# Kernel tuning notes

Measured on AMD Instinct MI355X. Metric: run time of the kernel, lower is better.

Reference implementation:

```python
import jax, jax.numpy as jnp
import numpy as np

GAMMA_EPS = 0.05
ALPHA_POS = 4.0
ALPHA_NEG = 1.0

N, D, K_CLUSTERS = 262144, 128, 256


def setup_inputs() -> dict:
    key = jax.random.key(0)
    k1, k2, k3 = jax.random.split(key, 3)
    Xemb = jax.random.normal(k1, (N, D), dtype=jnp.float32)
    scores = jax.random.normal(k2, (N, K_CLUSTERS), dtype=jnp.float32)
    labels = jax.random.randint(k3, (N,), 0, K_CLUSTERS, dtype=jnp.int64)
    h_bias = jnp.asarray(0.1, dtype=jnp.float32)  # nn.Parameter(init_bias)
    return {"Xemb": Xemb, "scores": scores, "labels": labels,
            "h_bias": h_bias, "K": K_CLUSTERS}


def _bcl_forward(Xemb, scores, h_bias, labels, K):
    # labels are uniform in [0, K), so sorted unique labels == arange(K)
    # and the loop's k-index equals the label itself (pos_idx = labels).
    bias = jax.nn.softplus(h_bias)
    pos_bias = bias
    neg_bias = 9.0 * bias + GAMMA_EPS

    # scatter-mean centroids per cluster, then L2-normalize each centroid
    sums = jax.ops.segment_sum(Xemb, labels, num_segments=K)          # [K, D]
    counts = jax.ops.segment_sum(jnp.ones((Xemb.shape[0],), Xemb.dtype),
                                 labels, num_segments=K)              # [K]
    centroids = sums / counts[:, None]
    centroids = centroids / jnp.linalg.norm(centroids, axis=1, keepdims=True)

    x2 = jnp.sum(Xemb * Xemb, axis=1, keepdims=True)                  # [N, 1]
    c2 = jnp.sum(centroids * centroids, axis=1)                       # [K]
    XC_dist = x2 + c2[None, :] - 2.0 * (Xemb @ centroids.T)           # [N, K]

    # positive distance: gather own-cluster column
    pos_distances = jnp.take_along_axis(XC_dist, labels[:, None], axis=1)[:, 0]
    pos_sample_loss = jax.nn.relu(pos_distances - pos_bias)

    # min over negative clusters (exclude own column)
    own = jax.nn.one_hot(labels, K, dtype=jnp.bool_)
    min_neg = jnp.min(jnp.where(own, jnp.inf, XC_dist), axis=1)
    neg_sample_loss = jax.nn.relu(neg_bias - min_neg)

    pos_loss = jnp.mean(pos_sample_loss) * ALPHA_POS
    neg_loss = jnp.mean(neg_sample_loss) * ALPHA_NEG
    return jnp.stack([pos_loss, neg_loss])  # [ctrd_pos, ctrd_neg]


def reference(Xemb, scores, labels, h_bias, K):
    return _bcl_forward(Xemb, scores, h_bias, labels, K)
```

## Files before the change

kernel.cpp:

```cpp
#include <hip/hip_runtime.h>
#include <hip/hip_bf16.h>

#define DD 128
#define KK 256
#define TS 256
#define ROWB 136
#define SPB1 1024

typedef __attribute__((ext_vector_type(8))) short short8;
typedef __attribute__((ext_vector_type(4))) float f32x4;

static __device__ __forceinline__ unsigned short f2bf(float f) {
    unsigned int u = __float_as_uint(f);
    return (unsigned short)((u + 0x7fffu + ((u >> 16) & 1u)) >> 16);
}
static __device__ __forceinline__ float bf2f(unsigned short h) {
    return __uint_as_float(((unsigned int)h) << 16);
}

template<int MODE>
__global__ __launch_bounds__(1024) void k_stage1_gather(
    const float* __restrict__ X, const int* __restrict__ labels,
    float* __restrict__ partial)
{
    __shared__ int lab[SPB1];
    __shared__ int idx[SPB1];
    __shared__ int hist[KK];
    __shared__ int start[KK + 1];
    __shared__ int cursor[KK];

    const int tid  = threadIdx.x;
    const int lane = tid & 63;
    const int wave = tid >> 6;
    const int base = blockIdx.x * SPB1;

    if (tid < KK) hist[tid] = 0;
    __syncthreads();
    {
        const int l = labels[base + tid];
        lab[tid] = l;
        atomicAdd(&hist[l], 1);
    }
    __syncthreads();
    if (wave == 0) {
        const int h0 = hist[4*lane], h1 = hist[4*lane+1];
        const int h2 = hist[4*lane+2], h3 = hist[4*lane+3];
        const int s = h0 + h1 + h2 + h3;
        int t = s;
#pragma unroll
        for (int d = 1; d < 64; d <<= 1) { const int u = __shfl_up(t, d); if (lane >= d) t += u; }
        const int e = t - s;
        start[4*lane]   = e;
        start[4*lane+1] = e + h0;
        start[4*lane+2] = e + h0 + h1;
        start[4*lane+3] = e + h0 + h1 + h2;
        if (lane == 63) start[KK] = t;
    }
    __syncthreads();
    if (tid < KK) cursor[tid] = start[tid];
    __syncthreads();
    {
        const int pos = atomicAdd(&cursor[lab[tid]], 1);
        idx[pos] = tid;
    }
    __syncthreads();

    const int c1 = (wave << 4) + 16;
    int c = wave << 4;
    const int s0 = start[c], s1 = start[c1];
    const int cnt = s1 - s0;

    float2 pf[8];
#pragma unroll
    for (int j = 0; j < 8; ++j)
        if (j < cnt)
            pf[j] = *(const float2*)(X + (size_t)(base + idx[s0 + j]) * DD + 2 * lane);

    float2 acc = make_float2(0.f, 0.f);
    int i = 0;
    for (; i + 8 <= cnt; i += 8) {
#pragma unroll
        for (int j = 0; j < 8; ++j) {
            const float2 v = pf[j];
            if (i + j + 8 < cnt)
                pf[j] = *(const float2*)(X + (size_t)(base + idx[s0 + i + j + 8]) * DD + 2 * lane);
            while (s0 + i + j >= start[c + 1]) {
                if (MODE == 2) {
                    atomicAdd(&partial[(size_t)c * DD + 2*lane],     acc.x);
                    atomicAdd(&partial[(size_t)c * DD + 2*lane + 1], acc.y);
                } else {
                    *(float2*)(partial + ((size_t)blockIdx.x * KK + c) * DD + 2*lane) = acc;
                }
                acc = make_float2(0.f, 0.f); ++c;
            }
            acc.x += v.x; acc.y += v.y;
        }
    }
#pragma unroll
    for (int j = 0; j < 8; ++j) {
        if (i + j < cnt) {
            const float2 v = pf[j];
            while (s0 + i + j >= start[c + 1]) {
                if (MODE == 2) {
                    atomicAdd(&partial[(size_t)c * DD + 2*lane],     acc.x);
                    atomicAdd(&partial[(size_t)c * DD + 2*lane + 1], acc.y);
                } else {
                    *(float2*)(partial + ((size_t)blockIdx.x * KK + c) * DD + 2*lane) = acc;
                }
                acc = make_float2(0.f, 0.f); ++c;
            }
            acc.x += v.x; acc.y += v.y;
        }
    }
    while (c < c1) {
        if (MODE == 2) {
            atomicAdd(&partial[(size_t)c * DD + 2*lane],     acc.x);
            atomicAdd(&partial[(size_t)c * DD + 2*lane + 1], acc.y);
        } else {
            *(float2*)(partial + ((size_t)blockIdx.x * KK + c) * DD + 2*lane) = acc;
        }
        acc = make_float2(0.f, 0.f); ++c;
    }
}

__global__ void k_stage2(const float* __restrict__ partial, int nparts,
                         unsigned short* __restrict__ centb)
{
    const int k = blockIdx.x;
    const int t = threadIdx.x;
    const int d = t & (DD - 1);
    const int slice = t >> 7;
    float s = 0.f;
    for (int b = slice; b < nparts; b += 4)
        s += partial[((size_t)b * KK + k) * DD + d];
    __shared__ float red[4][DD];
    red[slice][d] = s;
    __syncthreads();
    float v = 0.f;
    if (t < DD) v = red[0][d] + red[1][d] + red[2][d] + red[3][d];
    float sq = v * v;
#pragma unroll
    for (int m = 32; m > 0; m >>= 1) sq += __shfl_xor(sq, m);
    __shared__ float wsum[8];
    if ((t & 63) == 0) wsum[t >> 6] = sq;
    __syncthreads();
    if (t < DD) centb[k * DD + d] = f2bf(v * rsqrtf(wsum[0] + wsum[1]));
}

__global__ __launch_bounds__(1024, 4) void k_stage3(
    const float* __restrict__ Xf, const int* __restrict__ labels,
    const unsigned short* __restrict__ centb,
    const float* __restrict__ hbias, float* __restrict__ loss, int spb)
{
    __shared__ unsigned short Cl[KK * ROWB];
    __shared__ unsigned short Xl[TS * ROWB];
    __shared__ int   labs[TS];
    __shared__ float lred[32];

    const int tid = threadIdx.x;
    const float hb = *hbias;
    const float bias = (hb > 20.f) ? hb : log1pf(__expf(hb));
    const float pos_bias = bias;
    const float neg_bias = 9.f * bias + 0.05f;

    const uint4* csrc = (const uint4*)centb;
    for (int c = tid; c < KK * DD / 8; c += 1024) {
        const int row = c >> 4;
        const int col = (c & 15) << 3;
        *(uint4*)(&Cl[row * ROWB + col]) = csrc[c];
    }

    const int lane = tid & 63;
    const int wave = tid >> 6;
    const int m15  = lane & 15;
    const int q    = lane >> 4;
    const int kq   = q << 3;
    const int base = blockIdx.x * spb;
    float pos_acc = 0.f, neg_acc = 0.f;

    for (int t0 = 0; t0 < spb; t0 += TS) {
        __syncthreads();
        const float4* xsrc = (const float4*)(Xf + (size_t)(base + t0) * DD);
        for (int c = tid; c < TS * DD / 4; c += 1024) {
            const int row = c >> 5;
            const int col = (c & 31) << 2;
            const float4 v = xsrc[c];
            ushort4 pk = make_ushort4(f2bf(v.x), f2bf(v.y), f2bf(v.z), f2bf(v.w));
            *(ushort4*)(&Xl[row * ROWB + col]) = pk;
        }
        if (tid < TS) labs[tid] = labels[base + t0 + tid];
        __syncthreads();

        short8 afrag[4];
        const int arow = (wave << 4) + m15;
#pragma unroll
        for (int s = 0; s < 4; ++s)
            afrag[s] = *(const short8*)(&Xl[arow * ROWB + (s << 5) + kq]);

        float x2p = 0.f;
#pragma unroll
        for (int s = 0; s < 4; ++s)
#pragma unroll
            for (int j = 0; j < 8; ++j) {
                const float e = bf2f((unsigned short)afrag[s][j]);
                x2p = fmaf(e, e, x2p);
            }
        x2p += __shfl_xor(x2p, 16);
        x2p += __shfl_xor(x2p, 32);

        f32x4 acc[16];
#pragma unroll
        for (int t = 0; t < 16; ++t) acc[t] = (f32x4){0.f, 0.f, 0.f, 0.f};
#pragma unroll
        for (int t = 0; t < 16; ++t) {
            const int brow = (t << 4) + m15;
#pragma unroll
            for (int s = 0; s < 4; ++s) {
                const short8 bfrag = *(const short8*)(&Cl[brow * ROWB + (s << 5) + kq]);
                acc[t] = __builtin_amdgcn_mfma_f32_16x16x32_bf16(afrag[s], bfrag, acc[t], 0, 0, 0);
            }
        }

#pragma unroll
        for (int r = 0; r < 4; ++r) {
            const int ml = (wave << 4) + (q << 2) + r;
            const int l  = labs[ml];
            const float x2 = __shfl(x2p, (q << 2) + r, 16);
            float posd = -1e30f, negd = -1e30f;
#pragma unroll
            for (int t = 0; t < 16; ++t) {
                const int cl = (t << 4) + m15;
                const float v = acc[t][r];
                const bool isp = (cl == l);
                posd = isp ? v : posd;
                negd = isp ? negd : fmaxf(negd, v);
            }
#pragma unroll
            for (int m = 1; m < 16; m <<= 1) {
                posd = fmaxf(posd, __shfl_xor(posd, m));
                negd = fmaxf(negd, __shfl_xor(negd, m));
            }
            if (m15 == 0) {
                const float pd = x2 + 1.0f - 2.f * posd;
                const float nd = x2 + 1.0f - 2.f * negd;
                pos_acc += fmaxf(pd - pos_bias, 0.f);
                neg_acc += fmaxf(neg_bias - nd, 0.f);
            }
        }
    }

#pragma unroll
    for (int m = 32; m > 0; m >>= 1) {
        pos_acc += __shfl_xor(pos_acc, m);
        neg_acc += __shfl_xor(neg_acc, m);
    }
    if (lane == 0) { lred[wave] = pos_acc; lred[16 + wave] = neg_acc; }
    __syncthreads();
    if (tid == 0) {
        float p = 0.f, n = 0.f;
#pragma unroll
        for (int w = 0; w < 16; ++w) { p += lred[w]; n += lred[16 + w]; }
        atomicAdd(&loss[0], p);
        atomicAdd(&loss[1], n);
    }
}

__global__ void k_final(const float* __restrict__ loss, float* __restrict__ out, float invN)
{
    if (threadIdx.x == 0) {
        out[0] = 4.0f * loss[0] * invN;
        out[1] = loss[1] * invN;
    }
}

extern "C" void kernel_launch(void* const* d_in, const int* in_sizes, int n_in,
                              void* d_out, int out_size, void* d_ws, size_t ws_size,
                              hipStream_t stream)
{
    const float* X      = (const float*)d_in[0];
    const int*   labels = (const int*)d_in[2];
    const float* hbias  = (const float*)d_in[3];
    float* out = (float*)d_out;
    const int N = in_sizes[0] / DD;
    const int G = N / SPB1;

    char* ws = (char*)d_ws;
    const size_t offC    = 256;
    const size_t offPart = offC + (size_t)KK * DD * 2;
    const size_t szPart  = (size_t)G * KK * DD * 4;

    float*          loss    = (float*)ws;
    unsigned short* centb   = (unsigned short*)(ws + offC);
    float*          partial = (float*)(ws + offPart);

    const int mode   = (ws_size >= offPart + szPart) ? 0 : 2;
    const int nparts = (mode == 2) ? 1 : G;

    hipMemsetAsync(loss, 0, 2 * sizeof(float), stream);
    if (mode == 2) hipMemsetAsync(partial, 0, (size_t)KK * DD * 4, stream);

    if (mode == 0) k_stage1_gather<0><<<G, 1024, 0, stream>>>(X, labels, partial);
    else           k_stage1_gather<2><<<G, 1024, 0, stream>>>(X, labels, partial);

    k_stage2<<<KK, 512, 0, stream>>>(partial, nparts, centb);

    k_stage3<<<G, 1024, 0, stream>>>(X, labels, centb, hbias, loss, N / G);

    k_final<<<1, 64, 0, stream>>>(loss, out, 1.0f / (float)N);
}
```

Before: 466.0 us.

## Load X fragments directly from global with register prefetch, dropping LDS staging

```diff
diff --git a/kernel.cpp b/kernel.cpp
--- a/kernel.cpp
+++ b/kernel.cpp
@@ -69,6 +69,7 @@
     int c = wave << 4;
     const int s0 = start[c], s1 = start[c1];
     const int cnt = s1 - s0;
+    int nx = start[c + 1];
 
     float2 pf[8];
 #pragma unroll
@@ -84,14 +85,14 @@
             const float2 v = pf[j];
             if (i + j + 8 < cnt)
                 pf[j] = *(const float2*)(X + (size_t)(base + idx[s0 + i + j + 8]) * DD + 2 * lane);
-            while (s0 + i + j >= start[c + 1]) {
+            while (s0 + i + j >= nx) {
                 if (MODE == 2) {
                     atomicAdd(&partial[(size_t)c * DD + 2*lane],     acc.x);
                     atomicAdd(&partial[(size_t)c * DD + 2*lane + 1], acc.y);
                 } else {
                     *(float2*)(partial + ((size_t)blockIdx.x * KK + c) * DD + 2*lane) = acc;
                 }
-                acc = make_float2(0.f, 0.f); ++c;
+                acc = make_float2(0.f, 0.f); ++c; nx = start[c + 1];
             }
             acc.x += v.x; acc.y += v.y;
         }
@@ -100,14 +101,14 @@
     for (int j = 0; j < 8; ++j) {
         if (i + j < cnt) {
             const float2 v = pf[j];
-            while (s0 + i + j >= start[c + 1]) {
+            while (s0 + i + j >= nx) {
                 if (MODE == 2) {
                     atomicAdd(&partial[(size_t)c * DD + 2*lane],     acc.x);
                     atomicAdd(&partial[(size_t)c * DD + 2*lane + 1], acc.y);
                 } else {
                     *(float2*)(partial + ((size_t)blockIdx.x * KK + c) * DD + 2*lane) = acc;
                 }
-                acc = make_float2(0.f, 0.f); ++c;
+                acc = make_float2(0.f, 0.f); ++c; nx = start[c + 1];
             }
             acc.x += v.x; acc.y += v.y;
         }
@@ -147,14 +148,43 @@
     if (t < DD) centb[k * DD + d] = f2bf(v * rsqrtf(wsum[0] + wsum[1]));
 }
 
+
+static __device__ __forceinline__ short8 cvt_pair(const f32x4 lo, const f32x4 hi, float& x2p) {
+    short8 r;
+#pragma unroll
+    for (int j = 0; j < 4; ++j) {
+        const unsigned short u = f2bf(lo[j]);
+        r[j] = (short)u;
+        const float e = bf2f(u);
+        x2p = fmaf(e, e, x2p);
+    }
+#pragma unroll
+    for (int j = 0; j < 4; ++j) {
+        const unsigned short u = f2bf(hi[j]);
+        r[4 + j] = (short)u;
+        const float e = bf2f(u);
+        x2p = fmaf(e, e, x2p);
+    }
+    return r;
+}
+
+static __device__ __forceinline__ void mfma_step(
+    f32x4* acc, const short8 afrag, const unsigned short* Cl,
+    const int m15, const int kq, const int s)
+{
+#pragma unroll
+    for (int t = 0; t < 16; ++t) {
+        const short8 bfrag = *(const short8*)(&Cl[((t << 4) + m15) * ROWB + (s << 5) + kq]);
+        acc[t] = __builtin_amdgcn_mfma_f32_16x16x32_bf16(afrag, bfrag, acc[t], 0, 0, 0);
+    }
+}
+
 __global__ __launch_bounds__(1024, 4) void k_stage3(
     const float* __restrict__ Xf, const int* __restrict__ labels,
     const unsigned short* __restrict__ centb,
     const float* __restrict__ hbias, float* __restrict__ loss, int spb)
 {
     __shared__ unsigned short Cl[KK * ROWB];
-    __shared__ unsigned short Xl[TS * ROWB];
-    __shared__ int   labs[TS];
     __shared__ float lred[32];
 
     const int tid = threadIdx.x;
@@ -169,6 +199,7 @@
         const int col = (c & 15) << 3;
         *(uint4*)(&Cl[row * ROWB + col]) = csrc[c];
     }
+    __syncthreads();
 
     const int lane = tid & 63;
     const int wave = tid >> 6;
@@ -178,53 +209,47 @@
     const int base = blockIdx.x * spb;
     float pos_acc = 0.f, neg_acc = 0.f;
 
+    const float* xp = Xf + (size_t)(base + (wave << 4) + m15) * DD + kq;
+
+    f32x4 pa0 = *(const f32x4*)(xp);
+    f32x4 pa1 = *(const f32x4*)(xp + 4);
+    f32x4 pb0, pb1;
+
     for (int t0 = 0; t0 < spb; t0 += TS) {
-        __syncthreads();
-        const float4* xsrc = (const float4*)(Xf + (size_t)(base + t0) * DD);
-        for (int c = tid; c < TS * DD / 4; c += 1024) {
-            const int row = c >> 5;
-            const int col = (c & 31) << 2;
-            const float4 v = xsrc[c];
-            ushort4 pk = make_ushort4(f2bf(v.x), f2bf(v.y), f2bf(v.z), f2bf(v.w));
-            *(ushort4*)(&Xl[row * ROWB + col]) = pk;
-        }
-        if (tid < TS) labs[tid] = labels[base + t0 + tid];
-        __syncthreads();
-
-        short8 afrag[4];
-        const int arow = (wave << 4) + m15;
-#pragma unroll
-        for (int s = 0; s < 4; ++s)
-            afrag[s] = *(const short8*)(&Xl[arow * ROWB + (s << 5) + kq]);
-
+        const float* xt = xp + (size_t)t0 * DD;
+        f32x4 acc[16];
+#pragma unroll
+        for (int t = 0; t < 16; ++t) acc[t] = (f32x4){0.f, 0.f, 0.f, 0.f};
         float x2p = 0.f;
-#pragma unroll
-        for (int s = 0; s < 4; ++s)
-#pragma unroll
-            for (int j = 0; j < 8; ++j) {
-                const float e = bf2f((unsigned short)afrag[s][j]);
-                x2p = fmaf(e, e, x2p);
-            }
+        short8 afrag;
+
+        afrag = cvt_pair(pa0, pa1, x2p);
+        pb0 = *(const f32x4*)(xt + 32);
+        pb1 = *(const f32x4*)(xt + 36);
+        mfma_step(acc, afrag, Cl, m15, kq, 0);
+        afrag = cvt_pair(pb0, pb1, x2p);
+        pa0 = *(const f32x4*)(xt + 64);
+        pa1 = *(const f32x4*)(xt + 68);
+        mfma_step(acc, afrag, Cl, m15, kq, 1);
+        afrag = cvt_pair(pa0, pa1, x2p);
+        pb0 = *(const f32x4*)(xt + 96);
+        pb1 = *(const f32x4*)(xt + 100);
+        mfma_step(acc, afrag, Cl, m15, kq, 2);
+        afrag = cvt_pair(pb0, pb1, x2p);
+        if (t0 + TS < spb) {
+            const float* xn = xt + (size_t)TS * DD;
+            pa0 = *(const f32x4*)(xn);
+            pa1 = *(const f32x4*)(xn + 4);
+        }
+        mfma_step(acc, afrag, Cl, m15, kq, 3);
+
         x2p += __shfl_xor(x2p, 16);
         x2p += __shfl_xor(x2p, 32);
 
-        f32x4 acc[16];
-#pragma unroll
-        for (int t = 0; t < 16; ++t) acc[t] = (f32x4){0.f, 0.f, 0.f, 0.f};
-#pragma unroll
-        for (int t = 0; t < 16; ++t) {
-            const int brow = (t << 4) + m15;
-#pragma unroll
-            for (int s = 0; s < 4; ++s) {
-                const short8 bfrag = *(const short8*)(&Cl[brow * ROWB + (s << 5) + kq]);
-                acc[t] = __builtin_amdgcn_mfma_f32_16x16x32_bf16(afrag[s], bfrag, acc[t], 0, 0, 0);
-            }
-        }
-
 #pragma unroll
         for (int r = 0; r < 4; ++r) {
             const int ml = (wave << 4) + (q << 2) + r;
-            const int l  = labs[ml];
+            const int l  = labels[base + t0 + ml];
             const float x2 = __shfl(x2p, (q << 2) + r, 16);
             float posd = -1e30f, negd = -1e30f;
 #pragma unroll
```

Result: slower. 705.4 us (+51.4%).

## Register-prefetch next X tile, reorder MFMA loop, and read labels directly

Applied to the files above, without the earlier changes.

```diff
diff --git a/kernel.cpp b/kernel.cpp
--- a/kernel.cpp
+++ b/kernel.cpp
@@ -69,6 +69,7 @@
     int c = wave << 4;
     const int s0 = start[c], s1 = start[c1];
     const int cnt = s1 - s0;
+    int nx = start[c + 1];
 
     float2 pf[8];
 #pragma unroll
@@ -84,14 +85,14 @@
             const float2 v = pf[j];
             if (i + j + 8 < cnt)
                 pf[j] = *(const float2*)(X + (size_t)(base + idx[s0 + i + j + 8]) * DD + 2 * lane);
-            while (s0 + i + j >= start[c + 1]) {
+            while (s0 + i + j >= nx) {
                 if (MODE == 2) {
                     atomicAdd(&partial[(size_t)c * DD + 2*lane],     acc.x);
                     atomicAdd(&partial[(size_t)c * DD + 2*lane + 1], acc.y);
                 } else {
                     *(float2*)(partial + ((size_t)blockIdx.x * KK + c) * DD + 2*lane) = acc;
                 }
-                acc = make_float2(0.f, 0.f); ++c;
+                acc = make_float2(0.f, 0.f); ++c; nx = start[c + 1];
             }
             acc.x += v.x; acc.y += v.y;
         }
@@ -100,14 +101,14 @@
     for (int j = 0; j < 8; ++j) {
         if (i + j < cnt) {
             const float2 v = pf[j];
-            while (s0 + i + j >= start[c + 1]) {
+            while (s0 + i + j >= nx) {
                 if (MODE == 2) {
                     atomicAdd(&partial[(size_t)c * DD + 2*lane],     acc.x);
                     atomicAdd(&partial[(size_t)c * DD + 2*lane + 1], acc.y);
                 } else {
                     *(float2*)(partial + ((size_t)blockIdx.x * KK + c) * DD + 2*lane) = acc;
                 }
-                acc = make_float2(0.f, 0.f); ++c;
+                acc = make_float2(0.f, 0.f); ++c; nx = start[c + 1];
             }
             acc.x += v.x; acc.y += v.y;
         }
@@ -154,7 +155,6 @@
 {
     __shared__ unsigned short Cl[KK * ROWB];
     __shared__ unsigned short Xl[TS * ROWB];
-    __shared__ int   labs[TS];
     __shared__ float lred[32];
 
     const int tid = threadIdx.x;
@@ -178,59 +178,67 @@
     const int base = blockIdx.x * spb;
     float pos_acc = 0.f, neg_acc = 0.f;
 
+    float4 r[8];
+    {
+        const float4* xsrc = (const float4*)(Xf + (size_t)base * DD);
+#pragma unroll
+        for (int k = 0; k < 8; ++k)
+            r[k] = xsrc[tid + (k << 10)];
+    }
+
     for (int t0 = 0; t0 < spb; t0 += TS) {
         __syncthreads();
-        const float4* xsrc = (const float4*)(Xf + (size_t)(base + t0) * DD);
-        for (int c = tid; c < TS * DD / 4; c += 1024) {
+#pragma unroll
+        for (int k = 0; k < 8; ++k) {
+            const int c = tid + (k << 10);
             const int row = c >> 5;
             const int col = (c & 31) << 2;
-            const float4 v = xsrc[c];
+            const float4 v = r[k];
             ushort4 pk = make_ushort4(f2bf(v.x), f2bf(v.y), f2bf(v.z), f2bf(v.w));
             *(ushort4*)(&Xl[row * ROWB + col]) = pk;
         }
-        if (tid < TS) labs[tid] = labels[base + t0 + tid];
+        if (t0 + TS < spb) {
+            const float4* xn = (const float4*)(Xf + (size_t)(base + t0 + TS) * DD);
+#pragma unroll
+            for (int k = 0; k < 8; ++k)
+                r[k] = xn[tid + (k << 10)];
+        }
         __syncthreads();
 
-        short8 afrag[4];
+        f32x4 acc[16];
+#pragma unroll
+        for (int t = 0; t < 16; ++t) acc[t] = (f32x4){0.f, 0.f, 0.f, 0.f};
+        float x2p = 0.f;
+
         const int arow = (wave << 4) + m15;
 #pragma unroll
-        for (int s = 0; s < 4; ++s)
-            afrag[s] = *(const short8*)(&Xl[arow * ROWB + (s << 5) + kq]);
-
-        float x2p = 0.f;
-#pragma unroll
-        for (int s = 0; s < 4; ++s)
+        for (int s = 0; s < 4; ++s) {
+            const short8 afrag = *(const short8*)(&Xl[arow * ROWB + (s << 5) + kq]);
 #pragma unroll
             for (int j = 0; j < 8; ++j) {
-                const float e = bf2f((unsigned short)afrag[s][j]);
+                const float e = bf2f((unsigned short)afrag[j]);
                 x2p = fmaf(e, e, x2p);
             }
+#pragma unroll
+            for (int t = 0; t < 16; ++t) {
+                const short8 bfrag = *(const short8*)(&Cl[((t << 4) + m15) * ROWB + (s << 5) + kq]);
+                acc[t] = __builtin_amdgcn_mfma_f32_16x16x32_bf16(afrag, bfrag, acc[t], 0, 0, 0);
+            }
+        }
+
         x2p += __shfl_xor(x2p, 16);
         x2p += __shfl_xor(x2p, 32);
 
-        f32x4 acc[16];
-#pragma unroll
-        for (int t = 0; t < 16; ++t) acc[t] = (f32x4){0.f, 0.f, 0.f, 0.f};
-#pragma unroll
-        for (int t = 0; t < 16; ++t) {
-            const int brow = (t << 4) + m15;
-#pragma unroll
-            for (int s = 0; s < 4; ++s) {
-                const short8 bfrag = *(const short8*)(&Cl[brow * ROWB + (s << 5) + kq]);
-                acc[t] = __builtin_amdgcn_mfma_f32_16x16x32_bf16(afrag[s], bfrag, acc[t], 0, 0, 0);
-            }
-        }
-
-#pragma unroll
-        for (int r = 0; r < 4; ++r) {
-            const int ml = (wave << 4) + (q << 2) + r;
-            const int l  = labs[ml];
-            const float x2 = __shfl(x2p, (q << 2) + r, 16);
+#pragma unroll
+        for (int r4 = 0; r4 < 4; ++r4) {
+            const int ml = (wave << 4) + (q << 2) + r4;
+            const int l  = labels[base + t0 + ml];
+            const float x2 = __shfl(x2p, (q << 2) + r4, 16);
             float posd = -1e30f, negd = -1e30f;
 #pragma unroll
             for (int t = 0; t < 16; ++t) {
                 const int cl = (t << 4) + m15;
-                const float v = acc[t][r];
+                const float v = acc[t][r4];
                 const bool isp = (cl == l);
                 posd = isp ? v : posd;
                 negd = isp ? negd : fmaxf(negd, v);
```

Result: slower. 531.9 us (+14.1%).

## Replace counting-sort gather with shared-memory atomic centroid accumulation

Applied to the files above, without the earlier changes.

```diff
diff --git a/kernel.cpp b/kernel.cpp
--- a/kernel.cpp
+++ b/kernel.cpp
@@ -19,107 +19,43 @@
 }
 
 template<int MODE>
-__global__ __launch_bounds__(1024) void k_stage1_gather(
+__global__ __launch_bounds__(1024) void k_stage1_accum(
     const float* __restrict__ X, const int* __restrict__ labels,
     float* __restrict__ partial)
 {
-    __shared__ int lab[SPB1];
-    __shared__ int idx[SPB1];
-    __shared__ int hist[KK];
-    __shared__ int start[KK + 1];
-    __shared__ int cursor[KK];
+    __shared__ float Csh[KK * DD];
+    __shared__ int   labs_s[SPB1];
 
     const int tid  = threadIdx.x;
     const int lane = tid & 63;
     const int wave = tid >> 6;
     const int base = blockIdx.x * SPB1;
 
-    if (tid < KK) hist[tid] = 0;
-    __syncthreads();
-    {
-        const int l = labels[base + tid];
-        lab[tid] = l;
-        atomicAdd(&hist[l], 1);
-    }
-    __syncthreads();
-    if (wave == 0) {
-        const int h0 = hist[4*lane], h1 = hist[4*lane+1];
-        const int h2 = hist[4*lane+2], h3 = hist[4*lane+3];
-        const int s = h0 + h1 + h2 + h3;
-        int t = s;
-#pragma unroll
-        for (int d = 1; d < 64; d <<= 1) { const int u = __shfl_up(t, d); if (lane >= d) t += u; }
-        const int e = t - s;
-        start[4*lane]   = e;
-        start[4*lane+1] = e + h0;
-        start[4*lane+2] = e + h0 + h1;
-        start[4*lane+3] = e + h0 + h1 + h2;
-        if (lane == 63) start[KK] = t;
-    }
-    __syncthreads();
-    if (tid < KK) cursor[tid] = start[tid];
-    __syncthreads();
-    {
-        const int pos = atomicAdd(&cursor[lab[tid]], 1);
-        idx[pos] = tid;
-    }
-    __syncthreads();
-
-    const int c1 = (wave << 4) + 16;
-    int c = wave << 4;
-    const int s0 = start[c], s1 = start[c1];
-    const int cnt = s1 - s0;
-
-    float2 pf[8];
-#pragma unroll
-    for (int j = 0; j < 8; ++j)
-        if (j < cnt)
-            pf[j] = *(const float2*)(X + (size_t)(base + idx[s0 + j]) * DD + 2 * lane);
-
-    float2 acc = make_float2(0.f, 0.f);
-    int i = 0;
-    for (; i + 8 <= cnt; i += 8) {
-#pragma unroll
-        for (int j = 0; j < 8; ++j) {
-            const float2 v = pf[j];
-            if (i + j + 8 < cnt)
-                pf[j] = *(const float2*)(X + (size_t)(base + idx[s0 + i + j + 8]) * DD + 2 * lane);
-            while (s0 + i + j >= start[c + 1]) {
-                if (MODE == 2) {
-                    atomicAdd(&partial[(size_t)c * DD + 2*lane],     acc.x);
-                    atomicAdd(&partial[(size_t)c * DD + 2*lane + 1], acc.y);
-                } else {
-                    *(float2*)(partial + ((size_t)blockIdx.x * KK + c) * DD + 2*lane) = acc;
-                }
-                acc = make_float2(0.f, 0.f); ++c;
-            }
-            acc.x += v.x; acc.y += v.y;
-        }
-    }
-#pragma unroll
-    for (int j = 0; j < 8; ++j) {
-        if (i + j < cnt) {
-            const float2 v = pf[j];
-            while (s0 + i + j >= start[c + 1]) {
-                if (MODE == 2) {
-                    atomicAdd(&partial[(size_t)c * DD + 2*lane],     acc.x);
-                    atomicAdd(&partial[(size_t)c * DD + 2*lane + 1], acc.y);
-                } else {
-                    *(float2*)(partial + ((size_t)blockIdx.x * KK + c) * DD + 2*lane) = acc;
-                }
-                acc = make_float2(0.f, 0.f); ++c;
-            }
-            acc.x += v.x; acc.y += v.y;
-        }
-    }
-    while (c < c1) {
-        if (MODE == 2) {
-            atomicAdd(&partial[(size_t)c * DD + 2*lane],     acc.x);
-            atomicAdd(&partial[(size_t)c * DD + 2*lane + 1], acc.y);
-        } else {
-            *(float2*)(partial + ((size_t)blockIdx.x * KK + c) * DD + 2*lane) = acc;
-        }
-        acc = make_float2(0.f, 0.f); ++c;
+#pragma unroll
+    for (int i = 0; i < KK * DD / 1024; ++i)
+        Csh[tid + (i << 10)] = 0.f;
+    labs_s[tid] = labels[base + tid];
+    __syncthreads();
+
+    const float2* X2 = (const float2*)(X + (size_t)base * DD);
+#pragma unroll 4
+    for (int r = wave; r < SPB1; r += 16) {
+        const float2 v = X2[(size_t)r * 64 + lane];
+        const int l = labs_s[r];
+        atomicAdd(&Csh[l * DD + 2 * lane],     v.x);
+        atomicAdd(&Csh[l * DD + 2 * lane + 1], v.y);
+    }
+    __syncthreads();
+
+    if (MODE == 2) {
+        for (int i = tid; i < KK * DD; i += 1024)
+            atomicAdd(&partial[i], Csh[i]);
+    } else {
+        float4* dst = (float4*)(partial + (size_t)blockIdx.x * KK * DD);
+        const float4* src = (const float4*)Csh;
+#pragma unroll
+        for (int i = 0; i < KK * DD / 4 / 1024; ++i)
+            dst[tid + (i << 10)] = src[tid + (i << 10)];
     }
 }
 
@@ -299,8 +235,8 @@
     hipMemsetAsync(loss, 0, 2 * sizeof(float), stream);
     if (mode == 2) hipMemsetAsync(partial, 0, (size_t)KK * DD * 4, stream);
 
-    if (mode == 0) k_stage1_gather<0><<<G, 1024, 0, stream>>>(X, labels, partial);
-    else           k_stage1_gather<2><<<G, 1024, 0, stream>>>(X, labels, partial);
+    if (mode == 0) k_stage1_accum<0><<<G, 1024, 0, stream>>>(X, labels, partial);
+    else           k_stage1_accum<2><<<G, 1024, 0, stream>>>(X, labels, partial);
 
     k_stage2<<<KK, 512, 0, stream>>>(partial, nparts, centb);
 
```

Result: slower. 575.8 us (+23.6%).
